# Optimization experiments

Measured on AMD Instinct MI355X. Metric: run time of the kernel, lower is better.

Reference implementation:

```python
import jax, jax.numpy as jnp
import numpy as np

ROTARY_DIM = 128
ROTARY_BASE = 10000.0
ATTN_SCALE = 11.313708498984761  # sqrt(d_head=128)
N_HEADS = 16
N_KV = 4


def _apply_rotary(x, rotary_dim, rotary_base):
    # x: [seq, heads, d_head]
    seq_len = x.shape[0]
    dim_pairs = rotary_dim // 2
    freqs = 1.0 / rotary_base ** (jnp.arange(dim_pairs, dtype=jnp.float32) / dim_pairs)
    angles = jnp.outer(jnp.arange(seq_len), freqs)  # [seq, pairs]
    cos = jnp.cos(angles)[:, None, :]
    sin = jnp.sin(angles)[:, None, :]
    x_rot = x[..., :rotary_dim]
    x_pass = x[..., rotary_dim:]
    x1 = x_rot[..., ::2]
    x2 = x_rot[..., 1::2]
    out1 = x1 * cos - x2 * sin
    out2 = x1 * sin + x2 * cos
    rotated = jnp.stack([out1, out2], axis=-1).reshape(x_rot.shape)
    return jnp.concatenate([rotated, x_pass], axis=-1)


def setup_inputs() -> dict:
    key = jax.random.key(0)
    ks = jax.random.split(key, 5)
    seq, d_model, d_head = 4096, 2048, 128
    scale = 1.0 / np.sqrt(d_model)
    return {
        "x": jax.random.normal(ks[0], (seq, d_model), jnp.float32),
        "W_Q": jax.random.normal(ks[1], (N_HEADS, d_model, d_head), jnp.float32) * scale,
        "W_K": jax.random.normal(ks[2], (N_KV, d_model, d_head), jnp.float32) * scale,
        "W_V": jax.random.normal(ks[3], (N_KV, d_model, d_head), jnp.float32) * scale,
        "W_O": jax.random.normal(ks[4], (N_HEADS, d_head, d_model), jnp.float32) * scale,
        "b_Q": jnp.zeros((N_HEADS, d_head), jnp.float32),
        "b_K": jnp.zeros((N_KV, d_head), jnp.float32),
        "b_V": jnp.zeros((N_KV, d_head), jnp.float32),
        "b_O": jnp.zeros((2048,), jnp.float32),
    }


def reference(x, W_Q, W_K, W_V, W_O, b_Q, b_K, b_V, b_O):
    seq_len = x.shape[0]
    q = jnp.einsum('sm,nmh->snh', x, W_Q) + b_Q  # [s, 16, 128]
    k = jnp.einsum('sm,nmh->snh', x, W_K) + b_K  # [s, 4, 128]
    v = jnp.einsum('sm,nmh->snh', x, W_V) + b_V
    q = _apply_rotary(q, ROTARY_DIM, ROTARY_BASE)
    k = _apply_rotary(k, ROTARY_DIM, ROTARY_BASE)
    repeats = N_HEADS // N_KV
    k = jnp.repeat(k, repeats, axis=1)
    v = jnp.repeat(v, repeats, axis=1)
    attn_scores = jnp.einsum('qnh,knh->nqk', q, k) / ATTN_SCALE
    mask = jnp.tril(jnp.ones((seq_len, seq_len), dtype=jnp.bool_))
    attn_scores = jnp.where(mask[None, :, :], attn_scores,
                            jnp.finfo(attn_scores.dtype).min)
    pattern = jax.nn.softmax(attn_scores, axis=-1)
    z = jnp.einsum('nqk,knh->qnh', pattern, v)
    return jnp.einsum('snh,nhm->sm', z, W_O) + b_O
```

## Files before the change

kernel.cpp:

```cpp
#include <hip/hip_runtime.h>
#include <hip/hip_bf16.h>
#include <cstdint>
#include <cstddef>

#define SEQ    4096
#define DM     2048
#define DH     128
#define NH     16
#define NKV    4
#define NC     3072
#define KOFF   2048
#define VOFF   2560
#define Q_SCALE 0.12751730f

using bf16 = __hip_bfloat16;
typedef __bf16 bf16x8 __attribute__((ext_vector_type(8)));
typedef float f32x4 __attribute__((ext_vector_type(4)));
typedef float f32x16 __attribute__((ext_vector_type(16)));

static __device__ inline float bf2f(bf16 x) { return __bfloat162float(x); }
static __device__ inline bf16 f2bf(float x) { return __float2bfloat16(x); }

static __device__ inline void load_lds16(const bf16* g, bf16* l) {
    __builtin_amdgcn_global_load_lds(
        (const __attribute__((address_space(1))) uint32_t*)g,
        (__attribute__((address_space(3))) uint32_t*)l, 16, 0, 0);
}

__global__ void xconv(const float* __restrict__ in, bf16* __restrict__ out) {
    int i = blockIdx.x * 256 + threadIdx.x;
    float4 v = ((const float4*)in)[i];
    bf16 a = f2bf(v.x), b = f2bf(v.y), c = f2bf(v.z), d = f2bf(v.w);
    ushort4 u;
    u.x = *(unsigned short*)&a; u.y = *(unsigned short*)&b;
    u.z = *(unsigned short*)&c; u.w = *(unsigned short*)&d;
    ((ushort4*)out)[i] = u;
}

__global__ void prep_wqkv(const float* __restrict__ WQ, const float* __restrict__ WK,
                          const float* __restrict__ WV, bf16* __restrict__ wt) {
    __shared__ float tl[64][65];
    const int t = threadIdx.x;
    const int m0 = (int)blockIdx.x * 64;
    const int head = (int)blockIdx.y >> 1;
    const int h0 = ((int)blockIdx.y & 1) * 64;
    const float* src = (head < 16) ? WQ + (size_t)head * DM * DH
                     : (head < 20) ? WK + (size_t)(head - 16) * DM * DH
                                   : WV + (size_t)(head - 20) * DM * DH;
    {
        const int r = t >> 2, c = (t & 3) * 16;
        const float* p = src + (size_t)(m0 + r) * DH + h0 + c;
        #pragma unroll
        for (int kk = 0; kk < 4; ++kk) {
            float4 v = *(const float4*)(p + kk * 4);
            tl[r][c + kk * 4 + 0] = v.x; tl[r][c + kk * 4 + 1] = v.y;
            tl[r][c + kk * 4 + 2] = v.z; tl[r][c + kk * 4 + 3] = v.w;
        }
    }
    __syncthreads();
    {
        const int hh = t >> 2, ms = (t & 3) * 16;
        const int j = head * 128 + h0 + hh;
        bf16 tmp[16];
        #pragma unroll
        for (int i = 0; i < 16; ++i) tmp[i] = f2bf(tl[ms + i][hh]);
        bf16* q = wt + (size_t)j * DM + m0 + ms;
        *(bf16x8*)q       = *(bf16x8*)&tmp[0];
        *(bf16x8*)(q + 8) = *(bf16x8*)&tmp[8];
    }
}

__global__ void prep_wo(const float* __restrict__ WO, bf16* __restrict__ wt) {
    __shared__ float tl[64][65];
    const int t = threadIdx.x;
    const int m0 = (int)blockIdx.x * 64;
    const int j0 = (int)blockIdx.y * 64;
    {
        const int r = t >> 2, c = (t & 3) * 16;
        const float* p = WO + (size_t)(m0 + r) * DM + j0 + c;
        #pragma unroll
        for (int kk = 0; kk < 4; ++kk) {
            float4 v = *(const float4*)(p + kk * 4);
            tl[r][c + kk * 4 + 0] = v.x; tl[r][c + kk * 4 + 1] = v.y;
            tl[r][c + kk * 4 + 2] = v.z; tl[r][c + kk * 4 + 3] = v.w;
        }
    }
    __syncthreads();
    {
        const int hh = t >> 2, ms = (t & 3) * 16;
        bf16 tmp[16];
        #pragma unroll
        for (int i = 0; i < 16; ++i) tmp[i] = f2bf(tl[ms + i][hh]);
        bf16* q = wt + (size_t)(j0 + hh) * DM + m0 + ms;
        *(bf16x8*)q       = *(bf16x8*)&tmp[0];
        *(bf16x8*)(q + 8) = *(bf16x8*)&tmp[8];
    }
}

__global__ void prep_bias(const float* __restrict__ bQ, const float* __restrict__ bK,
                          const float* __restrict__ bV, float* __restrict__ bias) {
    int j = blockIdx.x * 256 + threadIdx.x;
    if (j >= NC) return;
    bias[j] = (j < KOFF) ? bQ[j] : (j < VOFF ? bK[j - KOFF] : bV[j - VOFF]);
}

__global__ void sctab(float2* __restrict__ tab) {
    int idx = blockIdx.x * 256 + threadIdx.x;
    int s = idx >> 6, i = idx & 63;
    float inv_freq = __expf(-(float)i * 0.14391156831212788f);
    float ang = (float)s * inv_freq;
    float2 cs;
    cs.x = cosf(ang);
    cs.y = sinf(ang);
    tab[idx] = cs;
}

#define BM 128
#define BN 128
#define BK 64

template <typename OutT, int ROT>
__global__ __launch_bounds__(256)
void gemm_bt(const bf16* __restrict__ A, const bf16* __restrict__ Bt,
             const float* __restrict__ bias, OutT* __restrict__ C, int N,
             const float2* __restrict__ tab) {
    __shared__ __align__(16) bf16 As[BM * BK];
    __shared__ __align__(16) bf16 Bs[BN * BK];
    const int tid = threadIdx.x;
    const int wave = tid >> 6, lane = tid & 63;
    const int quad = lane >> 4, l15 = lane & 15;
    const int wm = (wave >> 1) * 64, wn = (wave & 1) * 64;
    const int m0 = blockIdx.y * BM, n0 = blockIdx.x * BN;

    f32x4 acc[4][4] = {};

    const bf16* gsrc = (wave < 2)
        ? A  + (size_t)(m0 + (wave & 1) * 64) * DM
        : Bt + (size_t)(n0 + (wave & 1) * 64) * DM;
    bf16* lbase = (wave < 2 ? As : Bs) + (wave & 1) * 64 * BK;
    const int lrow = lane >> 3;
    const int gslot = (lane & 7) ^ lrow;
    const bf16* gp = gsrc + (size_t)lrow * DM + gslot * 8;

    const int rsw = l15 & 7;

    for (int k0 = 0; k0 < DM; k0 += BK) {
        __syncthreads();
        #pragma unroll
        for (int cc = 0; cc < 8; ++cc)
            load_lds16(gp + (size_t)cc * 8 * DM + k0, lbase + cc * 8 * BK);
        __syncthreads();

        #pragma unroll
        for (int ks = 0; ks < 2; ++ks) {
            bf16x8 af[4], bfr[4];
            #pragma unroll
            for (int i = 0; i < 4; ++i)
                af[i] = *(const bf16x8*)&As[(wm + i * 16 + l15) * BK + (((ks * 4 + quad) ^ rsw) * 8)];
            #pragma unroll
            for (int j = 0; j < 4; ++j)
                bfr[j] = *(const bf16x8*)&Bs[(wn + j * 16 + l15) * BK + (((ks * 4 + quad) ^ rsw) * 8)];
            #pragma unroll
            for (int i = 0; i < 4; ++i)
                #pragma unroll
                for (int j = 0; j < 4; ++j)
                    acc[i][j] = __builtin_amdgcn_mfma_f32_16x16x32_bf16(af[i], bfr[j], acc[i][j], 0, 0, 0);
        }
    }

    const bool doRot = ROT && (n0 < VOFF);
    const float scl = (n0 < KOFF) ? Q_SCALE : 1.0f;

    #pragma unroll
    for (int i = 0; i < 4; ++i) {
        int row = m0 + wm + i * 16 + quad * 4;
        #pragma unroll
        for (int j = 0; j < 4; ++j) {
            int col = n0 + wn + j * 16 + l15;
            float bv = bias[col];
            if (ROT && doRot) {
                const int ii = (col >> 1) & 63;
                const bool odd = col & 1;
                #pragma unroll
                for (int r = 0; r < 4; ++r) {
                    float v = acc[i][j][r] + bv;
                    float pv = __shfl_xor(v, 1);
                    float2 cs = tab[((row + r) << 6) + ii];
                    float o = odd ? (pv * cs.y + v * cs.x) : (v * cs.x - pv * cs.y);
                    C[(size_t)(row + r) * N + col] = (OutT)f2bf(o * scl);
                }
            } else {
                #pragma unroll
                for (int r = 0; r < 4; ++r) {
                    float val = acc[i][j][r] + bv;
                    if constexpr (sizeof(OutT) == 2)
                        C[(size_t)(row + r) * N + col] = f2bf(val);
                    else
                        C[(size_t)(row + r) * N + col] = val;
                }
            }
        }
    }
}

__global__ void vtrans(const bf16* __restrict__ qkv, bf16* __restrict__ vt) {
    __shared__ bf16 tl[64][72];
    const int t = threadIdx.x;
    const int s0 = (int)(blockIdx.x >> 3) * 64;
    const int c0 = (int)(blockIdx.x & 7) * 64;
    {
        int r = t >> 2, cc = (t & 3) * 16;
        const bf16* p = qkv + (size_t)(s0 + r) * NC + VOFF + c0 + cc;
        *(bf16x8*)&tl[r][cc]     = *(const bf16x8*)p;
        *(bf16x8*)&tl[r][cc + 8] = *(const bf16x8*)(p + 8);
    }
    __syncthreads();
    {
        int dd = t >> 2, sc = (t & 3) * 16;
        int col = c0 + dd;
        bf16 tmp[16];
        #pragma unroll
        for (int j = 0; j < 16; ++j) tmp[j] = tl[sc + j][dd];
        bf16* q = vt + (size_t)col * SEQ + s0 + sc;
        *(bf16x8*)q       = *(bf16x8*)&tmp[0];
        *(bf16x8*)(q + 8) = *(bf16x8*)&tmp[8];
    }
}

__global__ __launch_bounds__(256, 3)
void flash(const bf16* __restrict__ qkv, const bf16* __restrict__ vt,
           bf16* __restrict__ z) {
    __shared__ char smem[33280];
    bf16*  Ks  = (bf16*)smem;
    bf16*  Vs  = (bf16*)(smem + 16384);
    float* lml = (float*)(smem + 32768);
    float* ob  = (float*)smem;

    const int tid = threadIdx.x;
    const int wave = tid >> 6, lane = tid & 63;
    const int l31 = lane & 31, lh = lane >> 5;
    const int ch = wave >> 1;
    const int kh = wave & 1;
    const int bx = blockIdx.x;
    const int qt = 127 - (bx >> 3);
    const int g = (bx >> 1) & 3;
    const int hp = bx & 1;
    const int r_base = qt * 32 + ch * 16;
    const int ktmax = qt >> 1;
    const int rsw = l31 & 7;

    const int krow0 = wave * 16 + (lane >> 4);
    const int krow1 = krow0 + 4;
    const bf16* kp0 = qkv + KOFF + g * DH + (size_t)krow0 * NC + (((lane & 15) ^ (krow0 & 7)) * 8);
    const bf16* kp1 = qkv + KOFF + g * DH + (size_t)krow1 * NC + (((lane & 15) ^ (krow1 & 7)) * 8);
    const int vdd0 = wave * 32 + (lane >> 3);
    const bf16* vp0 = vt + (size_t)(g * DH + vdd0) * SEQ + (((lane & 7) ^ ((lane >> 3) & 7)) * 8);

    bf16x8 qf[8];
    {
        const int qrow = r_base + (l31 & 15);
        const int head = g * 4 + hp * 2 + (l31 >> 4);
        const bf16* qp = qkv + (size_t)qrow * NC + head * DH + lh * 8;
        #pragma unroll
        for (int s = 0; s < 8; ++s)
            qf[s] = *(const bf16x8*)(qp + s * 16);
    }

    f32x16 o_acc[4] = {};
    float lsum = 0.0f;

    for (int kt = 0; kt <= ktmax; ++kt) {
        __syncthreads();
        load_lds16(kp0,                        Ks + (wave * 4 + 0) * 512);
        load_lds16(kp1,                        Ks + (wave * 4 + 1) * 512);
        load_lds16(kp0 + (size_t)8 * NC,       Ks + (wave * 4 + 2) * 512);
        load_lds16(kp1 + (size_t)8 * NC,       Ks + (wave * 4 + 3) * 512);
        load_lds16(vp0,                        Vs + (wave * 4 + 0) * 512);
        load_lds16(vp0 + (size_t)8 * SEQ,      Vs + (wave * 4 + 1) * 512);
        load_lds16(vp0 + (size_t)16 * SEQ,     Vs + (wave * 4 + 2) * 512);
        load_lds16(vp0 + (size_t)24 * SEQ,     Vs + (wave * 4 + 3) * 512);
        __syncthreads();
        kp0 += (size_t)64 * NC; kp1 += (size_t)64 * NC; vp0 += 64;

        const int key_min = kt * 64 + kh * 32;
        if (key_min <= r_base + 15) {
            f32x16 sacc = {};
            __builtin_amdgcn_s_setprio(1);
            #pragma unroll
            for (int s = 0; s < 8; ++s) {
                bf16x8 kb = *(const bf16x8*)&Ks[(kh * 32 + l31) * 128 + (((lh + 2 * s) ^ rsw) * 8)];
                sacc = __builtin_amdgcn_mfma_f32_32x32x16_bf16(kb, qf[s], sacc, 0, 0, 0);
            }
            __builtin_amdgcn_s_setprio(0);

            const bool needmask = (key_min + 31 > r_base);
            const int qrow = r_base + (l31 & 15);
            float e[16];
            if (needmask) {
                #pragma unroll
                for (int rg = 0; rg < 16; ++rg) {
                    const int keyg = key_min + (rg & 3) + 8 * (rg >> 2) + 4 * lh;
                    float sv = sacc[rg];
                    if (keyg > qrow) sv = -INFINITY;
                    e[rg] = exp2f(sv);
                }
            } else {
                #pragma unroll
                for (int rg = 0; rg < 16; ++rg)
                    e[rg] = exp2f(sacc[rg]);
            }
            {
                float t0 = (e[0] + e[1]) + (e[2] + e[3]);
                float t1 = (e[4] + e[5]) + (e[6] + e[7]);
                float t2 = (e[8] + e[9]) + (e[10] + e[11]);
                float t3 = (e[12] + e[13]) + (e[14] + e[15]);
                lsum += (t0 + t1) + (t2 + t3);
            }

            bf16x8 pa[2];
            #pragma unroll
            for (int s2 = 0; s2 < 2; ++s2) {
                uint32_t wA0, wA1, wB0, wB1;
                asm("v_cvt_pk_bf16_f32 %0, %1, %2" : "=v"(wA0) : "v"(e[8*s2+0]), "v"(e[8*s2+1]));
                asm("v_cvt_pk_bf16_f32 %0, %1, %2" : "=v"(wA1) : "v"(e[8*s2+2]), "v"(e[8*s2+3]));
                asm("v_cvt_pk_bf16_f32 %0, %1, %2" : "=v"(wB0) : "v"(e[8*s2+4]), "v"(e[8*s2+5]));
                asm("v_cvt_pk_bf16_f32 %0, %1, %2" : "=v"(wB1) : "v"(e[8*s2+6]), "v"(e[8*s2+7]));
                asm volatile("v_permlane32_swap_b32 %0, %1" : "+v"(wA0), "+v"(wB0));
                asm volatile("v_permlane32_swap_b32 %0, %1" : "+v"(wA1), "+v"(wB1));
                union { uint32_t u[4]; bf16x8 v; } cvt;
                cvt.u[0] = wA0; cvt.u[1] = wA1; cvt.u[2] = wB0; cvt.u[3] = wB1;
                pa[s2] = cvt.v;
            }

            __builtin_amdgcn_s_setprio(1);
            #pragma unroll
            for (int nt = 0; nt < 4; ++nt) {
                #pragma unroll
                for (int s2 = 0; s2 < 2; ++s2) {
                    bf16x8 vb = *(const bf16x8*)&Vs[(nt * 32 + l31) * 64 + (((kh * 4 + lh + 2 * s2) ^ rsw) * 8)];
                    o_acc[nt] = __builtin_amdgcn_mfma_f32_32x32x16_bf16(pa[s2], vb, o_acc[nt], 0, 0, 0);
                }
            }
            __builtin_amdgcn_s_setprio(0);
        }
    }

    float la = lsum, lb = lsum;
    asm volatile("v_permlane32_swap_b32 %0, %1" : "+v"(la), "+v"(lb));
    const float l_tot = la + lb;

    __syncthreads();
    if (lh == 0) lml[wave * 32 + l31] = l_tot;
    if (kh == 1) {
        #pragma unroll
        for (int nt = 0; nt < 4; ++nt)
            #pragma unroll
            for (int rg = 0; rg < 16; ++rg) {
                const int m = (rg & 3) + 8 * (rg >> 2) + 4 * lh;
                ob[(ch * 32 + m) * 128 + nt * 32 + l31] = o_acc[nt][rg];
            }
    }
    __syncthreads();
    if (kh == 0) {
        float invl[16];
        #pragma unroll
        for (int rg = 0; rg < 16; ++rg) {
            const int m = (rg & 3) + 8 * (rg >> 2) + 4 * lh;
            invl[rg] = 1.0f / (lml[wave * 32 + m] + lml[(wave + 1) * 32 + m]);
        }
        #pragma unroll
        for (int nt = 0; nt < 4; ++nt)
            #pragma unroll
            for (int rg = 0; rg < 16; ++rg) {
                const int m = (rg & 3) + 8 * (rg >> 2) + 4 * lh;
                float oo = o_acc[nt][rg] + ob[(ch * 32 + m) * 128 + nt * 32 + l31];
                const int row = r_base + (m & 15);
                const int col = (g * 4 + hp * 2 + (m >> 4)) * DH + nt * 32 + l31;
                z[(size_t)row * DM + col] = f2bf(oo * invl[rg]);
            }
    }
}

extern "C" void kernel_launch(void* const* d_in, const int* in_sizes, int n_in,
                              void* d_out, int out_size, void* d_ws, size_t ws_size,
                              hipStream_t stream) {
    const float* x  = (const float*)d_in[0];
    const float* WQ = (const float*)d_in[1];
    const float* WK = (const float*)d_in[2];
    const float* WV = (const float*)d_in[3];
    const float* WO = (const float*)d_in[4];
    const float* bQ = (const float*)d_in[5];
    const float* bK = (const float*)d_in[6];
    const float* bV = (const float*)d_in[7];
    const float* bO = (const float*)d_in[8];
    float* out = (float*)d_out;

    char* ws = (char*)d_ws;
    bf16*  wt_cat = (bf16*)(ws);
    bf16*  wt_o   = (bf16*)(ws + 12582912);
    float* bias_c = (float*)(ws + 20971520);
    bf16*  qkv    = (bf16*)(ws + 20987904);
    bf16*  vt     = (bf16*)(ws + 46153728);
    bf16*  z      = (bf16*)(ws + 50348032);
    bf16*  xb     = (bf16*)(ws + 67125248);
    float2* sct   = (float2*)vt;

    xconv    <<<8192, 256, 0, stream>>>(x, xb);
    prep_wqkv<<<dim3(32, 48), 256, 0, stream>>>(WQ, WK, WV, wt_cat);
    prep_wo  <<<dim3(32, 32), 256, 0, stream>>>(WO, wt_o);
    prep_bias<<<12, 256, 0, stream>>>(bQ, bK, bV, bias_c);
    sctab    <<<1024, 256, 0, stream>>>(sct);
    gemm_bt<bf16, 1> <<<dim3(24, 32), 256, 0, stream>>>(xb, wt_cat, bias_c, qkv, NC, sct);
    vtrans   <<<512, 256, 0, stream>>>(qkv, vt);
    flash    <<<1024, 256, 0, stream>>>(qkv, vt, z);
    gemm_bt<float, 0><<<dim3(16, 32), 256, 0, stream>>>(z, wt_o, bO, out, DM, nullptr);
}
```

Baseline: 358.7 us.

## Replace GEMMs with 256x256 double-buffered 8-wave pipelined MFMA kernel

Swaps the 128x128 single-buffered GEMM for a 256x256-tile kernel with 8 waves, double-buffered LDS, and interleaved prefetch/compute phases with barriers and setprio. It aims to overlap global-to-LDS loads with MFMA work and raise arithmetic intensity per tile. The larger tiles shrink the grids to 192 and 128 blocks, which may underfill the CUs, and the 128KB LDS limits occupancy to one block per CU.

```diff
diff --git a/kernel.cpp b/kernel.cpp
--- a/kernel.cpp
+++ b/kernel.cpp
@@ -115,75 +115,153 @@
     tab[idx] = cs;
 }
 
-#define BM 128
-#define BN 128
-#define BK 64
+#define G8_NT (DM / 64)
 
 template <typename OutT, int ROT>
-__global__ __launch_bounds__(256)
-void gemm_bt(const bf16* __restrict__ A, const bf16* __restrict__ Bt,
-             const float* __restrict__ bias, OutT* __restrict__ C, int N,
-             const float2* __restrict__ tab) {
-    __shared__ __align__(16) bf16 As[BM * BK];
-    __shared__ __align__(16) bf16 Bs[BN * BK];
+__global__ __launch_bounds__(512, 2)
+void gemm8(const bf16* __restrict__ A, const bf16* __restrict__ Bt,
+           const float* __restrict__ bias, OutT* __restrict__ C, int N,
+           const float2* __restrict__ tab) {
+    __shared__ __align__(16) bf16 smem[65536];
     const int tid = threadIdx.x;
     const int wave = tid >> 6, lane = tid & 63;
     const int quad = lane >> 4, l15 = lane & 15;
-    const int wm = (wave >> 1) * 64, wn = (wave & 1) * 64;
-    const int m0 = blockIdx.y * BM, n0 = blockIdx.x * BN;
-
-    f32x4 acc[4][4] = {};
-
-    const bf16* gsrc = (wave < 2)
-        ? A  + (size_t)(m0 + (wave & 1) * 64) * DM
-        : Bt + (size_t)(n0 + (wave & 1) * 64) * DM;
-    bf16* lbase = (wave < 2 ? As : Bs) + (wave & 1) * 64 * BK;
+    const int wr = wave >> 2, wc = wave & 3;
+    const int m0 = blockIdx.y * 256, n0 = blockIdx.x * 256;
+    const int rsw = l15 & 7;
+
+    const int sw = wave & 3;
+    const bf16* gsrc = (wave < 4) ? A + (size_t)(m0 + sw * 64) * DM
+                                  : Bt + (size_t)(n0 + sw * 64) * DM;
     const int lrow = lane >> 3;
-    const int gslot = (lane & 7) ^ lrow;
-    const bf16* gp = gsrc + (size_t)lrow * DM + gslot * 8;
-
-    const int rsw = l15 & 7;
-
-    for (int k0 = 0; k0 < DM; k0 += BK) {
-        __syncthreads();
-        #pragma unroll
-        for (int cc = 0; cc < 8; ++cc)
-            load_lds16(gp + (size_t)cc * 8 * DM + k0, lbase + cc * 8 * BK);
-        __syncthreads();
-
-        #pragma unroll
-        for (int ks = 0; ks < 2; ++ks) {
-            bf16x8 af[4], bfr[4];
-            #pragma unroll
-            for (int i = 0; i < 4; ++i)
-                af[i] = *(const bf16x8*)&As[(wm + i * 16 + l15) * BK + (((ks * 4 + quad) ^ rsw) * 8)];
-            #pragma unroll
-            for (int j = 0; j < 4; ++j)
-                bfr[j] = *(const bf16x8*)&Bs[(wn + j * 16 + l15) * BK + (((ks * 4 + quad) ^ rsw) * 8)];
-            #pragma unroll
-            for (int i = 0; i < 4; ++i)
-                #pragma unroll
-                for (int j = 0; j < 4; ++j)
-                    acc[i][j] = __builtin_amdgcn_mfma_f32_16x16x32_bf16(af[i], bfr[j], acc[i][j], 0, 0, 0);
-        }
+    const bf16* gp = gsrc + (size_t)lrow * DM + (((lane & 7) ^ lrow) * 8);
+    bf16* sbase = smem + (wave < 4 ? 0 : 16384) + sw * 4096;
+
+    f32x4 acc[8][4] = {};
+
+    #pragma unroll
+    for (int c = 0; c < 8; ++c)
+        load_lds16(gp + (size_t)c * 8 * DM, sbase + c * 512);
+    __syncthreads();
+
+    #pragma unroll 1
+    for (int t = 0; t < G8_NT; ++t) {
+        const int cur = t & 1;
+        const bf16* Ab = smem + cur * 32768;
+        const bf16* Bb = Ab + 16384;
+        bf16* sdst = sbase + (cur ^ 1) * 32768;
+        const bool pf = (t + 1 < G8_NT);
+        const bf16* gpt = gp + (size_t)(t + 1) * 64;
+
+        bf16x8 aR[4][2], bR[2][2];
+
+        #pragma unroll
+        for (int mf = 0; mf < 4; ++mf)
+            #pragma unroll
+            for (int k = 0; k < 2; ++k)
+                aR[mf][k] = *(const bf16x8*)&Ab[(wr * 128 + mf * 16 + l15) * 64 + (((k * 4 + quad) ^ rsw) * 8)];
+        #pragma unroll
+        for (int nf = 0; nf < 2; ++nf)
+            #pragma unroll
+            for (int k = 0; k < 2; ++k)
+                bR[nf][k] = *(const bf16x8*)&Bb[(wc * 64 + nf * 16 + l15) * 64 + (((k * 4 + quad) ^ rsw) * 8)];
+        if (pf) { load_lds16(gpt + (size_t)0 * 8 * DM, sdst + 0 * 512);
+                  load_lds16(gpt + (size_t)1 * 8 * DM, sdst + 1 * 512); }
+        __builtin_amdgcn_s_barrier();
+        asm volatile("s_waitcnt lgkmcnt(0)" ::: "memory");
+        __builtin_amdgcn_sched_barrier(0);
+        __builtin_amdgcn_s_setprio(1);
+        #pragma unroll
+        for (int mf = 0; mf < 4; ++mf)
+            #pragma unroll
+            for (int nf = 0; nf < 2; ++nf)
+                #pragma unroll
+                for (int k = 0; k < 2; ++k)
+                    acc[mf][nf] = __builtin_amdgcn_mfma_f32_16x16x32_bf16(aR[mf][k], bR[nf][k], acc[mf][nf], 0, 0, 0);
+        __builtin_amdgcn_s_setprio(0);
+        __builtin_amdgcn_s_barrier();
+
+        #pragma unroll
+        for (int nf = 0; nf < 2; ++nf)
+            #pragma unroll
+            for (int k = 0; k < 2; ++k)
+                bR[nf][k] = *(const bf16x8*)&Bb[(wc * 64 + (2 + nf) * 16 + l15) * 64 + (((k * 4 + quad) ^ rsw) * 8)];
+        if (pf) { load_lds16(gpt + (size_t)2 * 8 * DM, sdst + 2 * 512);
+                  load_lds16(gpt + (size_t)3 * 8 * DM, sdst + 3 * 512); }
+        __builtin_amdgcn_s_barrier();
+        asm volatile("s_waitcnt lgkmcnt(0)" ::: "memory");
+        __builtin_amdgcn_sched_barrier(0);
+        __builtin_amdgcn_s_setprio(1);
+        #pragma unroll
+        for (int mf = 0; mf < 4; ++mf)
+            #pragma unroll
+            for (int nf = 0; nf < 2; ++nf)
+                #pragma unroll
+                for (int k = 0; k < 2; ++k)
+                    acc[mf][2 + nf] = __builtin_amdgcn_mfma_f32_16x16x32_bf16(aR[mf][k], bR[nf][k], acc[mf][2 + nf], 0, 0, 0);
+        __builtin_amdgcn_s_setprio(0);
+        __builtin_amdgcn_s_barrier();
+
+        #pragma unroll
+        for (int mf = 0; mf < 4; ++mf)
+            #pragma unroll
+            for (int k = 0; k < 2; ++k)
+                aR[mf][k] = *(const bf16x8*)&Ab[(wr * 128 + (4 + mf) * 16 + l15) * 64 + (((k * 4 + quad) ^ rsw) * 8)];
+        if (pf) { load_lds16(gpt + (size_t)4 * 8 * DM, sdst + 4 * 512);
+                  load_lds16(gpt + (size_t)5 * 8 * DM, sdst + 5 * 512); }
+        __builtin_amdgcn_s_barrier();
+        asm volatile("s_waitcnt lgkmcnt(0)" ::: "memory");
+        __builtin_amdgcn_sched_barrier(0);
+        __builtin_amdgcn_s_setprio(1);
+        #pragma unroll
+        for (int mf = 0; mf < 4; ++mf)
+            #pragma unroll
+            for (int nf = 0; nf < 2; ++nf)
+                #pragma unroll
+                for (int k = 0; k < 2; ++k)
+                    acc[4 + mf][2 + nf] = __builtin_amdgcn_mfma_f32_16x16x32_bf16(aR[mf][k], bR[nf][k], acc[4 + mf][2 + nf], 0, 0, 0);
+        __builtin_amdgcn_s_setprio(0);
+        __builtin_amdgcn_s_barrier();
+
+        #pragma unroll
+        for (int nf = 0; nf < 2; ++nf)
+            #pragma unroll
+            for (int k = 0; k < 2; ++k)
+                bR[nf][k] = *(const bf16x8*)&Bb[(wc * 64 + nf * 16 + l15) * 64 + (((k * 4 + quad) ^ rsw) * 8)];
+        if (pf) { load_lds16(gpt + (size_t)6 * 8 * DM, sdst + 6 * 512);
+                  load_lds16(gpt + (size_t)7 * 8 * DM, sdst + 7 * 512); }
+        __builtin_amdgcn_s_barrier();
+        asm volatile("s_waitcnt lgkmcnt(0)" ::: "memory");
+        __builtin_amdgcn_sched_barrier(0);
+        __builtin_amdgcn_s_setprio(1);
+        #pragma unroll
+        for (int mf = 0; mf < 4; ++mf)
+            #pragma unroll
+            for (int nf = 0; nf < 2; ++nf)
+                #pragma unroll
+                for (int k = 0; k < 2; ++k)
+                    acc[4 + mf][nf] = __builtin_amdgcn_mfma_f32_16x16x32_bf16(aR[mf][k], bR[nf][k], acc[4 + mf][nf], 0, 0, 0);
+        __builtin_amdgcn_s_setprio(0);
+        asm volatile("s_waitcnt vmcnt(0)" ::: "memory");
+        __builtin_amdgcn_sched_barrier(0);
+        __builtin_amdgcn_s_barrier();
     }
 
     const bool doRot = ROT && (n0 < VOFF);
     const float scl = (n0 < KOFF) ? Q_SCALE : 1.0f;
-
     #pragma unroll
-    for (int i = 0; i < 4; ++i) {
-        int row = m0 + wm + i * 16 + quad * 4;
-        #pragma unroll
-        for (int j = 0; j < 4; ++j) {
-            int col = n0 + wn + j * 16 + l15;
+    for (int mf = 0; mf < 8; ++mf) {
+        int row = m0 + wr * 128 + mf * 16 + quad * 4;
+        #pragma unroll
+        for (int nf = 0; nf < 4; ++nf) {
+            int col = n0 + wc * 64 + nf * 16 + l15;
             float bv = bias[col];
             if (ROT && doRot) {
                 const int ii = (col >> 1) & 63;
                 const bool odd = col & 1;
                 #pragma unroll
                 for (int r = 0; r < 4; ++r) {
-                    float v = acc[i][j][r] + bv;
+                    float v = acc[mf][nf][r] + bv;
                     float pv = __shfl_xor(v, 1);
                     float2 cs = tab[((row + r) << 6) + ii];
                     float o = odd ? (pv * cs.y + v * cs.x) : (v * cs.x - pv * cs.y);
@@ -192,7 +270,7 @@
             } else {
                 #pragma unroll
                 for (int r = 0; r < 4; ++r) {
-                    float val = acc[i][j][r] + bv;
+                    float val = acc[mf][nf][r] + bv;
                     if constexpr (sizeof(OutT) == 2)
                         C[(size_t)(row + r) * N + col] = f2bf(val);
                     else
@@ -410,8 +488,8 @@
     prep_wo  <<<dim3(32, 32), 256, 0, stream>>>(WO, wt_o);
     prep_bias<<<12, 256, 0, stream>>>(bQ, bK, bV, bias_c);
     sctab    <<<1024, 256, 0, stream>>>(sct);
-    gemm_bt<bf16, 1> <<<dim3(24, 32), 256, 0, stream>>>(xb, wt_cat, bias_c, qkv, NC, sct);
+    gemm8<bf16, 1> <<<dim3(12, 16), 512, 0, stream>>>(xb, wt_cat, bias_c, qkv, NC, sct);
     vtrans   <<<512, 256, 0, stream>>>(qkv, vt);
     flash    <<<1024, 256, 0, stream>>>(qkv, vt, z);
-    gemm_bt<float, 0><<<dim3(16, 32), 256, 0, stream>>>(z, wt_o, bO, out, DM, nullptr);
-}
+    gemm8<float, 0><<<dim3(8, 16), 512, 0, stream>>>(z, wt_o, bO, out, DM, nullptr);
+}
```

Result: slower. 366.8 us (+2.2%).

## Fuse V transpose into QKV GEMM epilogue and merge bias prep into sctab

Applied to the files above, without the earlier changes.

The QKV GEMM blocks that produce V columns now stage their bias-added tile in LDS and write it out transposed straight into the vt buffer. This removes the separate vtrans kernel and its read of V from qkv. The bias-concatenation kernel is also folded into the sin/cos table kernel, saving one more launch. The rotary table moves into the z buffer, since vt is now written during the GEMM. V is no longer written to qkv, so this is only correct if flash reads V solely from vt.

```diff
diff --git a/kernel.cpp b/kernel.cpp
--- a/kernel.cpp
+++ b/kernel.cpp
@@ -97,14 +97,9 @@
     }
 }
 
-__global__ void prep_bias(const float* __restrict__ bQ, const float* __restrict__ bK,
-                          const float* __restrict__ bV, float* __restrict__ bias) {
-    int j = blockIdx.x * 256 + threadIdx.x;
-    if (j >= NC) return;
-    bias[j] = (j < KOFF) ? bQ[j] : (j < VOFF ? bK[j - KOFF] : bV[j - VOFF]);
-}
-
-__global__ void sctab(float2* __restrict__ tab) {
+__global__ void sctab(float2* __restrict__ tab,
+                      const float* __restrict__ bQ, const float* __restrict__ bK,
+                      const float* __restrict__ bV, float* __restrict__ bias) {
     int idx = blockIdx.x * 256 + threadIdx.x;
     int s = idx >> 6, i = idx & 63;
     float inv_freq = __expf(-(float)i * 0.14391156831212788f);
@@ -113,19 +108,23 @@
     cs.x = cosf(ang);
     cs.y = sinf(ang);
     tab[idx] = cs;
+    if (idx < NC)
+        bias[idx] = (idx < KOFF) ? bQ[idx] : (idx < VOFF ? bK[idx - KOFF] : bV[idx - VOFF]);
 }
 
 #define BM 128
 #define BN 128
 #define BK 64
+#define VTL 132
 
 template <typename OutT, int ROT>
 __global__ __launch_bounds__(256)
 void gemm_bt(const bf16* __restrict__ A, const bf16* __restrict__ Bt,
              const float* __restrict__ bias, OutT* __restrict__ C, int N,
-             const float2* __restrict__ tab) {
-    __shared__ __align__(16) bf16 As[BM * BK];
-    __shared__ __align__(16) bf16 Bs[BN * BK];
+             const float2* __restrict__ tab, bf16* __restrict__ vtq) {
+    __shared__ __align__(16) char smemraw[33792];
+    bf16* As = (bf16*)smemraw;
+    bf16* Bs = (bf16*)(smemraw + 16384);
     const int tid = threadIdx.x;
     const int wave = tid >> 6, lane = tid & 63;
     const int quad = lane >> 4, l15 = lane & 15;
@@ -166,6 +165,38 @@
                 for (int j = 0; j < 4; ++j)
                     acc[i][j] = __builtin_amdgcn_mfma_f32_16x16x32_bf16(af[i], bfr[j], acc[i][j], 0, 0, 0);
         }
+    }
+
+    if (ROT && n0 >= VOFF) {
+        __syncthreads();
+        bf16* vtile = (bf16*)smemraw;
+        #pragma unroll
+        for (int i = 0; i < 4; ++i) {
+            const int rl0 = wm + i * 16 + quad * 4;
+            #pragma unroll
+            for (int j = 0; j < 4; ++j) {
+                const int cl = wn + j * 16 + l15;
+                const float bv = bias[n0 + cl];
+                ushort4 w;
+                bf16 h;
+                h = f2bf(acc[i][j][0] + bv); w.x = *(unsigned short*)&h;
+                h = f2bf(acc[i][j][1] + bv); w.y = *(unsigned short*)&h;
+                h = f2bf(acc[i][j][2] + bv); w.z = *(unsigned short*)&h;
+                h = f2bf(acc[i][j][3] + bv); w.w = *(unsigned short*)&h;
+                *(ushort4*)&vtile[cl * VTL + rl0] = w;
+            }
+        }
+        __syncthreads();
+        #pragma unroll
+        for (int p = 0; p < 4; ++p) {
+            const int c = p * 32 + (tid >> 3);
+            const int s = (tid & 7) * 16;
+            bf16* dst = vtq + (size_t)(n0 - VOFF + c) * SEQ + m0 + s;
+            const bf16* srcl = vtile + c * VTL + s;
+            *(bf16x8*)dst       = *(const bf16x8*)srcl;
+            *(bf16x8*)(dst + 8) = *(const bf16x8*)(srcl + 8);
+        }
+        return;
     }
 
     const bool doRot = ROT && (n0 < VOFF);
@@ -200,30 +231,6 @@
                 }
             }
         }
-    }
-}
-
-__global__ void vtrans(const bf16* __restrict__ qkv, bf16* __restrict__ vt) {
-    __shared__ bf16 tl[64][72];
-    const int t = threadIdx.x;
-    const int s0 = (int)(blockIdx.x >> 3) * 64;
-    const int c0 = (int)(blockIdx.x & 7) * 64;
-    {
-        int r = t >> 2, cc = (t & 3) * 16;
-        const bf16* p = qkv + (size_t)(s0 + r) * NC + VOFF + c0 + cc;
-        *(bf16x8*)&tl[r][cc]     = *(const bf16x8*)p;
-        *(bf16x8*)&tl[r][cc + 8] = *(const bf16x8*)(p + 8);
-    }
-    __syncthreads();
-    {
-        int dd = t >> 2, sc = (t & 3) * 16;
-        int col = c0 + dd;
-        bf16 tmp[16];
-        #pragma unroll
-        for (int j = 0; j < 16; ++j) tmp[j] = tl[sc + j][dd];
-        bf16* q = vt + (size_t)col * SEQ + s0 + sc;
-        *(bf16x8*)q       = *(bf16x8*)&tmp[0];
-        *(bf16x8*)(q + 8) = *(bf16x8*)&tmp[8];
     }
 }
 
@@ -403,15 +410,13 @@
     bf16*  vt     = (bf16*)(ws + 46153728);
     bf16*  z      = (bf16*)(ws + 50348032);
     bf16*  xb     = (bf16*)(ws + 67125248);
-    float2* sct   = (float2*)vt;
+    float2* sct   = (float2*)z;
 
     xconv    <<<8192, 256, 0, stream>>>(x, xb);
     prep_wqkv<<<dim3(32, 48), 256, 0, stream>>>(WQ, WK, WV, wt_cat);
     prep_wo  <<<dim3(32, 32), 256, 0, stream>>>(WO, wt_o);
-    prep_bias<<<12, 256, 0, stream>>>(bQ, bK, bV, bias_c);
-    sctab    <<<1024, 256, 0, stream>>>(sct);
-    gemm_bt<bf16, 1> <<<dim3(24, 32), 256, 0, stream>>>(xb, wt_cat, bias_c, qkv, NC, sct);
-    vtrans   <<<512, 256, 0, stream>>>(qkv, vt);
+    sctab    <<<1024, 256, 0, stream>>>(sct, bQ, bK, bV, bias_c);
+    gemm_bt<bf16, 1> <<<dim3(24, 32), 256, 0, stream>>>(xb, wt_cat, bias_c, qkv, NC, sct, vt);
     flash    <<<1024, 256, 0, stream>>>(qkv, vt, z);
-    gemm_bt<float, 0><<<dim3(16, 32), 256, 0, stream>>>(z, wt_o, bO, out, DM, nullptr);
-}
+    gemm_bt<float, 0><<<dim3(16, 32), 256, 0, stream>>>(z, wt_o, bO, out, DM, nullptr, nullptr);
+}
```

After: 342.0 us. -4.6%, faster.
